# Kernel tuning notes

Measured on AMD Instinct MI355X. Metric: run time of the kernel, lower is better.

## Reference

```python
import jax, jax.numpy as jnp
import numpy as np

B, N, D, C, S = 128, 100000, 256, 2000, 751  # batch, memory size, feat dim, num classes, source classes
TEMP = 0.05
EPS = 1e-06


def _l2norm(x):
    return x / jnp.linalg.norm(x, axis=-1, keepdims=True)


def setup_inputs() -> dict:
    key = jax.random.key(0)
    k1, k2, k3, k4, k5 = jax.random.split(key, 5)
    inputs = _l2norm(jax.random.normal(k1, (B, D), dtype=jnp.float32))
    inputs2 = _l2norm(jax.random.normal(k2, (B, D), dtype=jnp.float32))
    features = _l2norm(jax.random.normal(k3, (N, D), dtype=jnp.float32))
    labels = jax.random.randint(k4, (N,), 0, C)
    labels = labels.at[:C].set(jnp.arange(C))  # ensure labels.max()+1 == C
    indexes = jax.random.randint(k5, (B,), 0, N)
    return {"inputs": inputs, "inputs2": inputs2, "features": features,
            "labels": labels, "indexes": indexes, "source_classes": S}


def reference(inputs, inputs2, features, labels, indexes, source_classes):
    # memory-bank logits, [B, N]
    logits = (inputs @ features.T) / TEMP
    logits2 = (inputs2 @ features.T) / TEMP
    targets = labels[indexes]  # [B]

    # per-class counts and segment-mean of logits over the bank, [C, B]
    nums = jax.ops.segment_sum(jnp.ones((N,), jnp.float32), labels, num_segments=C)  # [C]
    denom = jnp.where(nums > 0, nums, 1.0)[:, None]  # [C, 1]
    sim = jax.ops.segment_sum(logits.T, labels, num_segments=C) / denom   # [C, B]
    sim2 = jax.ops.segment_sum(logits2.T, labels, num_segments=C) / denom  # [C, B]

    # MSE between class-probability maps over the first source_classes classes
    p1 = sim[:source_classes].T   # [B, S]
    p2 = sim2[:source_classes].T  # [B, S]
    diff = jax.nn.softmax(p1, axis=1) - jax.nn.softmax(p2, axis=1)
    loss_mse = jnp.sum(diff * diff) / source_classes

    # hard-positive/negative mining: per-class max of logits (0 for empty classes)
    seg_max = jax.ops.segment_max(logits.T, labels, num_segments=C)  # [C, B], -inf where empty
    present = (nums > 0)  # [C]
    sim_hard = jnp.where(present[:, None], seg_max, 0.0).T  # [B, C]
    # for the target class, use the hardest (min) positive instead
    seg_min = jax.ops.segment_min(logits.T, labels, num_segments=C)  # [C, B]
    b_idx = jnp.arange(B)
    sim_hard = sim_hard.at[b_idx, targets].set(seg_min[targets, b_idx])

    # masked softmax over present classes + NLL
    mask = present.astype(jnp.float32)[None, :]  # [1, C]
    exps = jnp.exp(sim_hard) * mask
    masked_sim = exps / (jnp.sum(exps, axis=1, keepdims=True) + EPS)
    loss_con = -jnp.mean(jnp.log(masked_sim[b_idx, targets] + EPS))

    return (loss_con, loss_mse)
```

## Files before the change

kernel.cpp:

```cpp
#include <hip/hip_runtime.h>
#include <hip/hip_bf16.h>

#define BB 128
#define NN 100000
#define DD 256
#define CC 2000
#define SS 751
#define INVTEMP 20.0f
#define EPSV 1e-6f

typedef __attribute__((ext_vector_type(8))) short bf16x8;
typedef __attribute__((ext_vector_type(8))) unsigned short u16x8;
typedef __attribute__((ext_vector_type(4))) float f32x4;

__device__ __forceinline__ unsigned short f2bf(float x) {
    unsigned int u = __float_as_uint(x);
    u += 0x7fffu + ((u >> 16) & 1u);
    return (unsigned short)(u >> 16);
}


__global__ void hist_kernel(const int* __restrict__ labels, int* __restrict__ counts) {
    int n = blockIdx.x * 256 + threadIdx.x;
    if (n < NN) atomicAdd(&counts[labels[n]], 1);
}

__global__ __launch_bounds__(256) void scan_kernel(const int* __restrict__ counts,
                                                   int* __restrict__ offsets,
                                                   int* __restrict__ cursor) {
    const int PT = 8;
    int tid = threadIdx.x;
    int vals[PT];
    int tot = 0;
    #pragma unroll
    for (int i = 0; i < PT; ++i) {
        int c = tid * PT + i;
        vals[i] = (c < CC) ? counts[c] : 0;
        tot += vals[i];
    }
    __shared__ int sh[256];
    sh[tid] = tot;
    __syncthreads();
    for (int ofs = 1; ofs < 256; ofs <<= 1) {
        int v = (tid >= ofs) ? sh[tid - ofs] : 0;
        __syncthreads();
        sh[tid] += v;
        __syncthreads();
    }
    int run = sh[tid] - tot;
    #pragma unroll
    for (int i = 0; i < PT; ++i) {
        int c = tid * PT + i;
        if (c < CC) { offsets[c] = run; cursor[c] = run; }
        run += vals[i];
    }
}

__global__ void scatter_kernel(const int* __restrict__ labels, int* __restrict__ cursor,
                               int* __restrict__ sorted_idx) {
    int n = blockIdx.x * 256 + threadIdx.x;
    if (n < NN) {
        int c = labels[n];
        int p = atomicAdd(&cursor[c], 1);
        sorted_idx[p] = n;
    }
}

__global__ void prep_inputs(const float* __restrict__ in1, const float* __restrict__ in2,
                            unsigned short* __restrict__ inb) {
    int ch = blockIdx.x * 256 + threadIdx.x;
    if (ch >= 8192) return;
    int l  = ch & 63;
    int kc = (ch >> 6) & 7;
    int nr = ch >> 9;
    int row = nr * 16 + (l & 15);
    const float* src = (row < BB) ? (in1 + (size_t)row * DD)
                                  : (in2 + (size_t)(row - BB) * DD);
    int k0 = kc * 32 + ((l >> 4) << 3);
    u16x8 o;
    #pragma unroll
    for (int j = 0; j < 8; ++j) o[j] = f2bf(src[k0 + j]);
    *(u16x8*)(inb + (size_t)ch * 8) = o;
}

__global__ __launch_bounds__(512) void class_mfma(
    const float* __restrict__ features, const unsigned short* __restrict__ inb,
    const int* __restrict__ offsets, const int* __restrict__ counts,
    const int* __restrict__ sorted_idx,
    float* __restrict__ gsumA, float* __restrict__ gsumB,
    float* __restrict__ gmax, float* __restrict__ gmin)
{
    const int c   = blockIdx.x;
    const int cnt = counts[c];
    const int off = offsets[c];
    const int tid = threadIdx.x;
    const int w   = tid >> 6;
    const int l   = tid & 63;

    __shared__ __align__(16) unsigned short a_lds[64 * 256];
    __shared__ int midx[64];
    char* lds_base = (char*)a_lds;

    float s_sum[2] = {0.f, 0.f};
    float s_max[2] = {-3.4e38f, -3.4e38f};
    float s_min[2] = { 3.4e38f,  3.4e38f};

    for (int base = 0; base < cnt; base += 64) {
        __syncthreads();
        if (tid < 64) {
            int j = base + tid;
            midx[tid] = (j < cnt) ? sorted_idx[off + j] : -1;
        }
        __syncthreads();

        #pragma unroll
        for (int i = 0; i < 4; ++i) {
            int m     = (tid + 512 * i) >> 5;
            int cslot = tid & 31;
            int n = midx[m];
            float4 v0 = make_float4(0.f, 0.f, 0.f, 0.f), v1 = v0;
            if (n >= 0) {
                const float4* src = (const float4*)(features + (size_t)n * DD + cslot * 8);
                v0 = src[0]; v1 = src[1];
            }
            u16x8 o;
            o[0] = f2bf(v0.x); o[1] = f2bf(v0.y); o[2] = f2bf(v0.z); o[3] = f2bf(v0.w);
            o[4] = f2bf(v1.x); o[5] = f2bf(v1.y); o[6] = f2bf(v1.z); o[7] = f2bf(v1.w);
            int byte = m * 512 + cslot * 16;
            byte ^= (m & 7) << 4;
            *(u16x8*)(lds_base + byte) = o;
        }
        __syncthreads();

        f32x4 acc[4][2];
        #pragma unroll
        for (int ma = 0; ma < 4; ++ma)
            #pragma unroll
            for (int nb = 0; nb < 2; ++nb)
                acc[ma][nb] = (f32x4){0.f, 0.f, 0.f, 0.f};

        #pragma unroll
        for (int kc = 0; kc < 8; ++kc) {
            bf16x8 a[4];
            #pragma unroll
            for (int ma = 0; ma < 4; ++ma) {
                int m = 16 * ma + (l & 15);
                int byte = m * 512 + kc * 64 + ((l >> 4) << 4);
                byte ^= (m & 7) << 4;
                a[ma] = *(const bf16x8*)(lds_base + byte);
            }
            bf16x8 b[2];
            #pragma unroll
            for (int nb = 0; nb < 2; ++nb) {
                int nr = 2 * w + nb;
                b[nb] = *(const bf16x8*)(inb + (((size_t)(nr * 8 + kc) * 64 + l) << 3));
            }
            #pragma unroll
            for (int ma = 0; ma < 4; ++ma)
                #pragma unroll
                for (int nb = 0; nb < 2; ++nb)
                    acc[ma][nb] = __builtin_amdgcn_mfma_f32_16x16x32_bf16(
                        a[ma], b[nb], acc[ma][nb], 0, 0, 0);
        }

        #pragma unroll
        for (int ma = 0; ma < 4; ++ma) {
            #pragma unroll
            for (int reg = 0; reg < 4; ++reg) {
                int member = base + 16 * ma + 4 * (l >> 4) + reg;
                if (member < cnt) {
                    #pragma unroll
                    for (int nb = 0; nb < 2; ++nb) {
                        float v = acc[ma][nb][reg] * INVTEMP;
                        s_sum[nb] += v;
                        s_max[nb] = fmaxf(s_max[nb], v);
                        s_min[nb] = fminf(s_min[nb], v);
                    }
                }
            }
        }
    }

    #pragma unroll
    for (int nb = 0; nb < 2; ++nb) {
        s_sum[nb] += __shfl_xor(s_sum[nb], 16);
        s_sum[nb] += __shfl_xor(s_sum[nb], 32);
        s_max[nb] = fmaxf(s_max[nb], __shfl_xor(s_max[nb], 16));
        s_max[nb] = fmaxf(s_max[nb], __shfl_xor(s_max[nb], 32));
        s_min[nb] = fminf(s_min[nb], __shfl_xor(s_min[nb], 16));
        s_min[nb] = fminf(s_min[nb], __shfl_xor(s_min[nb], 32));
    }
    if (l < 16) {
        #pragma unroll
        for (int nb = 0; nb < 2; ++nb) {
            int col = 32 * w + 16 * nb + l;
            if (col < BB) {
                gsumA[c * BB + col] = s_sum[nb];
                gmax[c * BB + col]  = s_max[nb];
                gmin[c * BB + col]  = s_min[nb];
            } else {
                gsumB[c * BB + (col - BB)] = s_sum[nb];
            }
        }
    }
}


__device__ __forceinline__ float blk_reduce_sum(float v) {
    __shared__ float sh[4];
    int lane = threadIdx.x & 63, w = threadIdx.x >> 6;
    #pragma unroll
    for (int o = 32; o; o >>= 1) v += __shfl_down(v, o, 64);
    __syncthreads();
    if (lane == 0) sh[w] = v;
    __syncthreads();
    return sh[0] + sh[1] + sh[2] + sh[3];
}

__device__ __forceinline__ float blk_reduce_max(float v) {
    __shared__ float sh[4];
    int lane = threadIdx.x & 63, w = threadIdx.x >> 6;
    #pragma unroll
    for (int o = 32; o; o >>= 1) v = fmaxf(v, __shfl_down(v, o, 64));
    __syncthreads();
    if (lane == 0) sh[w] = v;
    __syncthreads();
    return fmaxf(fmaxf(sh[0], sh[1]), fmaxf(sh[2], sh[3]));
}

__global__ __launch_bounds__(256) void finalize_kernel(
    const float* __restrict__ gsumA, const float* __restrict__ gsumB,
    const float* __restrict__ gmax, const float* __restrict__ gmin,
    const int* __restrict__ counts, const int* __restrict__ labels,
    const int* __restrict__ indexes, float* __restrict__ out)
{
    const int b   = blockIdx.x;
    const int tid = threadIdx.x;
    const int tgt = labels[indexes[b]];

    __shared__ float sh_etgt;
    float local = 0.f;
    for (int c = tid; c < CC; c += 256) {
        float v = (c == tgt) ? gmin[c * BB + b] : gmax[c * BB + b];
        float e = (counts[c] > 0) ? expf(v) : 0.f;
        local += e;
        if (c == tgt) sh_etgt = e;
    }
    float sum_e = blk_reduce_sum(local);
    float etgt = sh_etgt;
    float loss_con_b = -logf(etgt / (sum_e + EPSV) + EPSV);

    __shared__ float a1[SS], a2[SS];
    for (int c = tid; c < SS; c += 256) {
        int n = counts[c];
        float icnt = 1.f / (float)(n > 0 ? n : 1);
        a1[c] = gsumA[c * BB + b] * icnt;
        a2[c] = gsumB[c * BB + b] * icnt;
    }
    __syncthreads();
    float m1 = -3.4e38f, m2 = -3.4e38f;
    for (int c = tid; c < SS; c += 256) { m1 = fmaxf(m1, a1[c]); m2 = fmaxf(m2, a2[c]); }
    m1 = blk_reduce_max(m1);
    m2 = blk_reduce_max(m2);
    float s1 = 0.f, s2 = 0.f;
    for (int c = tid; c < SS; c += 256) { s1 += expf(a1[c] - m1); s2 += expf(a2[c] - m2); }
    s1 = blk_reduce_sum(s1);
    s2 = blk_reduce_sum(s2);
    float inv1 = 1.f / s1, inv2 = 1.f / s2;
    float dsum = 0.f;
    for (int c = tid; c < SS; c += 256) {
        float d = expf(a1[c] - m1) * inv1 - expf(a2[c] - m2) * inv2;
        dsum += d * d;
    }
    dsum = blk_reduce_sum(dsum);
    if (tid == 0) {
        atomicAdd(&out[0], loss_con_b * (1.0f / (float)BB));
        atomicAdd(&out[1], dsum * (1.0f / (float)SS));
    }
}


extern "C" void kernel_launch(void* const* d_in, const int* in_sizes, int n_in,
                              void* d_out, int out_size, void* d_ws, size_t ws_size,
                              hipStream_t stream) {
    const float* inputs   = (const float*)d_in[0];
    const float* inputs2  = (const float*)d_in[1];
    const float* features = (const float*)d_in[2];
    const int*   labels   = (const int*)d_in[3];
    const int*   indexes  = (const int*)d_in[4];

    float* out = (float*)d_out;

    int* wsi     = (int*)d_ws;
    int* counts  = wsi;
    int* offsets = wsi + 2048;
    int* cursor  = wsi + 4096;
    int* sorted  = wsi + 6144;
    unsigned short* inb = (unsigned short*)(wsi + 106144);
    float* gsumA = (float*)d_ws + 138912;
    float* gsumB = gsumA + CC * BB;
    float* gmaxp = gsumB + CC * BB;
    float* gminp = gmaxp + CC * BB;

    hipMemsetAsync(counts, 0, 2048 * sizeof(int), stream);
    hipMemsetAsync(d_out, 0, 2 * sizeof(float), stream);

    hist_kernel<<<(NN + 255) / 256, 256, 0, stream>>>(labels, counts);
    scan_kernel<<<1, 256, 0, stream>>>(counts, offsets, cursor);
    scatter_kernel<<<(NN + 255) / 256, 256, 0, stream>>>(labels, cursor, sorted);
    prep_inputs<<<32, 256, 0, stream>>>(inputs, inputs2, inb);
    class_mfma<<<CC, 512, 0, stream>>>(features, inb, offsets, counts, sorted,
                                       gsumA, gsumB, gmaxp, gminp);
    finalize_kernel<<<BB, 256, 0, stream>>>(gsumA, gsumB, gmaxp, gminp, counts,
                                            labels, indexes, out);
}
```

Measured before the change: 110.7 us.

## Split class blocks by input half, preload B fragments, fuse hist/prep kernels

Launches two 256-thread blocks per class, one for inputs and one for inputs2, instead of a single 512-thread block, so the bank rows are gathered twice but there are twice as many blocks. B fragments are hoisted into registers once per block rather than reloaded every chunk. Half 1 accumulates sums directly in MFMA accumulators across chunks, and the temperature scale is moved to the end. Histogram and input prep are fused into one launch, and the output memset moves into the scan kernel. Together these cut launches and per-chunk overhead, at the cost of double feature gather traffic and more register pressure.

```diff
diff --git a/kernel.cpp b/kernel.cpp
--- a/kernel.cpp
+++ b/kernel.cpp
@@ -9,6 +9,9 @@
 #define INVTEMP 20.0f
 #define EPSV 1e-6f
 
+#define HIST_BLOCKS 391
+#define PREP_BLOCKS 32
+
 typedef __attribute__((ext_vector_type(8))) short bf16x8;
 typedef __attribute__((ext_vector_type(8))) unsigned short u16x8;
 typedef __attribute__((ext_vector_type(4))) float f32x4;
@@ -19,17 +22,39 @@
     return (unsigned short)(u >> 16);
 }
 
-
-__global__ void hist_kernel(const int* __restrict__ labels, int* __restrict__ counts) {
-    int n = blockIdx.x * 256 + threadIdx.x;
-    if (n < NN) atomicAdd(&counts[labels[n]], 1);
+__global__ __launch_bounds__(256) void hist_prep_kernel(
+    const int* __restrict__ labels, int* __restrict__ counts,
+    const float* __restrict__ in1, const float* __restrict__ in2,
+    unsigned short* __restrict__ inb)
+{
+    int bid = blockIdx.x;
+    if (bid < HIST_BLOCKS) {
+        int n = bid * 256 + threadIdx.x;
+        if (n < NN) atomicAdd(&counts[labels[n]], 1);
+    } else {
+        int ch = (bid - HIST_BLOCKS) * 256 + threadIdx.x;
+        if (ch >= 8192) return;
+        int l  = ch & 63;
+        int kc = (ch >> 6) & 7;
+        int nr = ch >> 9;
+        int row = nr * 16 + (l & 15);
+        const float* src = (row < BB) ? (in1 + (size_t)row * DD)
+                                      : (in2 + (size_t)(row - BB) * DD);
+        int k0 = kc * 32 + ((l >> 4) << 3);
+        u16x8 o;
+        #pragma unroll
+        for (int j = 0; j < 8; ++j) o[j] = f2bf(src[k0 + j]);
+        *(u16x8*)(inb + (size_t)ch * 8) = o;
+    }
 }
 
 __global__ __launch_bounds__(256) void scan_kernel(const int* __restrict__ counts,
                                                    int* __restrict__ offsets,
-                                                   int* __restrict__ cursor) {
+                                                   int* __restrict__ cursor,
+                                                   float* __restrict__ out) {
     const int PT = 8;
     int tid = threadIdx.x;
+    if (tid == 0) { out[0] = 0.f; out[1] = 0.f; }
     int vals[PT];
     int tot = 0;
     #pragma unroll
@@ -66,31 +91,16 @@
     }
 }
 
-__global__ void prep_inputs(const float* __restrict__ in1, const float* __restrict__ in2,
-                            unsigned short* __restrict__ inb) {
-    int ch = blockIdx.x * 256 + threadIdx.x;
-    if (ch >= 8192) return;
-    int l  = ch & 63;
-    int kc = (ch >> 6) & 7;
-    int nr = ch >> 9;
-    int row = nr * 16 + (l & 15);
-    const float* src = (row < BB) ? (in1 + (size_t)row * DD)
-                                  : (in2 + (size_t)(row - BB) * DD);
-    int k0 = kc * 32 + ((l >> 4) << 3);
-    u16x8 o;
-    #pragma unroll
-    for (int j = 0; j < 8; ++j) o[j] = f2bf(src[k0 + j]);
-    *(u16x8*)(inb + (size_t)ch * 8) = o;
-}
-
-__global__ __launch_bounds__(512) void class_mfma(
+__global__ __launch_bounds__(256) void class_mfma(
     const float* __restrict__ features, const unsigned short* __restrict__ inb,
     const int* __restrict__ offsets, const int* __restrict__ counts,
     const int* __restrict__ sorted_idx,
     float* __restrict__ gsumA, float* __restrict__ gsumB,
     float* __restrict__ gmax, float* __restrict__ gmin)
 {
-    const int c   = blockIdx.x;
+    const int bid = blockIdx.x;
+    const int c   = bid >> 1;
+    const int h   = bid & 1;
     const int cnt = counts[c];
     const int off = offsets[c];
     const int tid = threadIdx.x;
@@ -98,28 +108,40 @@
     const int l   = tid & 63;
 
     __shared__ __align__(16) unsigned short a_lds[64 * 256];
-    __shared__ int midx[64];
     char* lds_base = (char*)a_lds;
+
+    bf16x8 bfr[16];
+    #pragma unroll
+    for (int kc = 0; kc < 8; ++kc) {
+        #pragma unroll
+        for (int nb = 0; nb < 2; ++nb) {
+            int nr = h * 8 + 2 * w + nb;
+            bfr[kc * 2 + nb] = *(const bf16x8*)(inb + (((size_t)(nr * 8 + kc) * 64 + l) << 3));
+        }
+    }
 
     float s_sum[2] = {0.f, 0.f};
     float s_max[2] = {-3.4e38f, -3.4e38f};
     float s_min[2] = { 3.4e38f,  3.4e38f};
 
+    f32x4 acc[4][2];
+    #pragma unroll
+    for (int ma = 0; ma < 4; ++ma)
+        #pragma unroll
+        for (int nb = 0; nb < 2; ++nb)
+            acc[ma][nb] = (f32x4){0.f, 0.f, 0.f, 0.f};
+
     for (int base = 0; base < cnt; base += 64) {
         __syncthreads();
-        if (tid < 64) {
-            int j = base + tid;
-            midx[tid] = (j < cnt) ? sorted_idx[off + j] : -1;
-        }
-        __syncthreads();
-
-        #pragma unroll
-        for (int i = 0; i < 4; ++i) {
-            int m     = (tid + 512 * i) >> 5;
+
+        #pragma unroll
+        for (int i = 0; i < 8; ++i) {
+            int m     = 8 * i + (tid >> 5);
             int cslot = tid & 31;
-            int n = midx[m];
+            int gm    = base + m;
             float4 v0 = make_float4(0.f, 0.f, 0.f, 0.f), v1 = v0;
-            if (n >= 0) {
+            if (gm < cnt) {
+                int n = sorted_idx[off + gm];
                 const float4* src = (const float4*)(features + (size_t)n * DD + cslot * 8);
                 v0 = src[0]; v1 = src[1];
             }
@@ -132,12 +154,13 @@
         }
         __syncthreads();
 
-        f32x4 acc[4][2];
-        #pragma unroll
-        for (int ma = 0; ma < 4; ++ma)
+        if (h == 0) {
             #pragma unroll
-            for (int nb = 0; nb < 2; ++nb)
-                acc[ma][nb] = (f32x4){0.f, 0.f, 0.f, 0.f};
+            for (int ma = 0; ma < 4; ++ma)
+                #pragma unroll
+                for (int nb = 0; nb < 2; ++nb)
+                    acc[ma][nb] = (f32x4){0.f, 0.f, 0.f, 0.f};
+        }
 
         #pragma unroll
         for (int kc = 0; kc < 8; ++kc) {
@@ -149,57 +172,80 @@
                 byte ^= (m & 7) << 4;
                 a[ma] = *(const bf16x8*)(lds_base + byte);
             }
-            bf16x8 b[2];
-            #pragma unroll
-            for (int nb = 0; nb < 2; ++nb) {
-                int nr = 2 * w + nb;
-                b[nb] = *(const bf16x8*)(inb + (((size_t)(nr * 8 + kc) * 64 + l) << 3));
-            }
             #pragma unroll
             for (int ma = 0; ma < 4; ++ma)
                 #pragma unroll
                 for (int nb = 0; nb < 2; ++nb)
                     acc[ma][nb] = __builtin_amdgcn_mfma_f32_16x16x32_bf16(
-                        a[ma], b[nb], acc[ma][nb], 0, 0, 0);
-        }
-
-        #pragma unroll
-        for (int ma = 0; ma < 4; ++ma) {
+                        a[ma], bfr[kc * 2 + nb], acc[ma][nb], 0, 0, 0);
+        }
+
+        if (h == 0) {
+            if (base + 64 <= cnt) {
+                #pragma unroll
+                for (int ma = 0; ma < 4; ++ma)
+                    #pragma unroll
+                    for (int reg = 0; reg < 4; ++reg)
+                        #pragma unroll
+                        for (int nb = 0; nb < 2; ++nb) {
+                            float v = acc[ma][nb][reg];
+                            s_sum[nb] += v;
+                            s_max[nb] = fmaxf(s_max[nb], v);
+                            s_min[nb] = fminf(s_min[nb], v);
+                        }
+            } else {
+                int mb = base + 4 * (l >> 4);
+                #pragma unroll
+                for (int ma = 0; ma < 4; ++ma)
+                    #pragma unroll
+                    for (int reg = 0; reg < 4; ++reg) {
+                        bool valid = (mb + 16 * ma + reg) < cnt;
+                        #pragma unroll
+                        for (int nb = 0; nb < 2; ++nb) {
+                            float v = acc[ma][nb][reg];
+                            s_sum[nb] += v;
+                            s_max[nb] = valid ? fmaxf(s_max[nb], v) : s_max[nb];
+                            s_min[nb] = valid ? fminf(s_min[nb], v) : s_min[nb];
+                        }
+                    }
+            }
+        }
+    }
+
+    if (h == 1) {
+        #pragma unroll
+        for (int ma = 0; ma < 4; ++ma)
             #pragma unroll
-            for (int reg = 0; reg < 4; ++reg) {
-                int member = base + 16 * ma + 4 * (l >> 4) + reg;
-                if (member < cnt) {
-                    #pragma unroll
-                    for (int nb = 0; nb < 2; ++nb) {
-                        float v = acc[ma][nb][reg] * INVTEMP;
-                        s_sum[nb] += v;
-                        s_max[nb] = fmaxf(s_max[nb], v);
-                        s_min[nb] = fminf(s_min[nb], v);
-                    }
-                }
-            }
-        }
+            for (int reg = 0; reg < 4; ++reg)
+                #pragma unroll
+                for (int nb = 0; nb < 2; ++nb)
+                    s_sum[nb] += acc[ma][nb][reg];
     }
 
     #pragma unroll
     for (int nb = 0; nb < 2; ++nb) {
+        s_sum[nb] *= INVTEMP;
         s_sum[nb] += __shfl_xor(s_sum[nb], 16);
         s_sum[nb] += __shfl_xor(s_sum[nb], 32);
-        s_max[nb] = fmaxf(s_max[nb], __shfl_xor(s_max[nb], 16));
-        s_max[nb] = fmaxf(s_max[nb], __shfl_xor(s_max[nb], 32));
-        s_min[nb] = fminf(s_min[nb], __shfl_xor(s_min[nb], 16));
-        s_min[nb] = fminf(s_min[nb], __shfl_xor(s_min[nb], 32));
+        if (h == 0) {
+            s_max[nb] *= INVTEMP;
+            s_min[nb] *= INVTEMP;
+            s_max[nb] = fmaxf(s_max[nb], __shfl_xor(s_max[nb], 16));
+            s_max[nb] = fmaxf(s_max[nb], __shfl_xor(s_max[nb], 32));
+            s_min[nb] = fminf(s_min[nb], __shfl_xor(s_min[nb], 16));
+            s_min[nb] = fminf(s_min[nb], __shfl_xor(s_min[nb], 32));
+        }
     }
     if (l < 16) {
         #pragma unroll
         for (int nb = 0; nb < 2; ++nb) {
             int col = 32 * w + 16 * nb + l;
-            if (col < BB) {
+            if (h == 0) {
                 gsumA[c * BB + col] = s_sum[nb];
                 gmax[c * BB + col]  = s_max[nb];
                 gmin[c * BB + col]  = s_min[nb];
             } else {
-                gsumB[c * BB + (col - BB)] = s_sum[nb];
+                gsumB[c * BB + col] = s_sum[nb];
             }
         }
     }
@@ -303,14 +349,13 @@
     float* gminp = gmaxp + CC * BB;
 
     hipMemsetAsync(counts, 0, 2048 * sizeof(int), stream);
-    hipMemsetAsync(d_out, 0, 2 * sizeof(float), stream);
-
-    hist_kernel<<<(NN + 255) / 256, 256, 0, stream>>>(labels, counts);
-    scan_kernel<<<1, 256, 0, stream>>>(counts, offsets, cursor);
+
+    hist_prep_kernel<<<HIST_BLOCKS + PREP_BLOCKS, 256, 0, stream>>>(
+        labels, counts, inputs, inputs2, inb);
+    scan_kernel<<<1, 256, 0, stream>>>(counts, offsets, cursor, out);
     scatter_kernel<<<(NN + 255) / 256, 256, 0, stream>>>(labels, cursor, sorted);
-    prep_inputs<<<32, 256, 0, stream>>>(inputs, inputs2, inb);
-    class_mfma<<<CC, 512, 0, stream>>>(features, inb, offsets, counts, sorted,
-                                       gsumA, gsumB, gmaxp, gminp);
+    class_mfma<<<2 * CC, 256, 0, stream>>>(features, inb, offsets, counts, sorted,
+                                           gsumA, gsumB, gmaxp, gminp);
     finalize_kernel<<<BB, 256, 0, stream>>>(gsumA, gsumB, gmaxp, gminp, counts,
                                             labels, indexes, out);
 }
```

New measurement: 128.4 us. 1.16x slower.
